# Kernel optimization log

Measured on AMD Instinct MI355X. Metric: run time of the kernel, lower is better.

Reference implementation:

```python
import jax, jax.numpy as jnp
import numpy as np

KERNEL_SIZE = 11
SIGMA = 1.5
IN_CH = 2


def _gaussian_kernel(kernel_size: int, sigma: float) -> jnp.ndarray:
    start = (1 - kernel_size) / 2
    coords = jnp.arange(start, start + kernel_size, dtype=jnp.float32)
    k1d = jnp.exp(-((coords / sigma) ** 2) / 2)
    k1d = k1d / k1d.sum()
    k2d = jnp.outer(k1d, k1d)  # [K, K]
    # OIHW depthwise kernel: [out_ch=IN_CH, in_ch/groups=1, K, K]
    return jnp.broadcast_to(k2d, (IN_CH, 1, kernel_size, kernel_size))


def _blur(img: jnp.ndarray, kernel: jnp.ndarray) -> jnp.ndarray:
    pad = KERNEL_SIZE // 2
    return jax.lax.conv_general_dilated(
        img, kernel,
        window_strides=(1, 1),
        padding=[(pad, pad), (pad, pad)],
        dimension_numbers=("NCHW", "OIHW", "NCHW"),
        feature_group_count=IN_CH,
    )


def setup_inputs() -> dict:
    key = jax.random.key(0)
    kx, ky = jax.random.split(key)
    shape = (32, 2, 512, 512)
    x = jax.random.uniform(kx, shape, dtype=jnp.float32)
    y = jax.random.uniform(ky, shape, dtype=jnp.float32)
    return {"x": x, "y": y}


def reference(x, y):
    kernel = _gaussian_kernel(KERNEL_SIZE, SIGMA)
    ux = _blur(x, kernel)
    uy = _blur(y, kernel)
    uxx = _blur(x * x, kernel)
    uyy = _blur(y * y, kernel)
    uxy = _blur(x * y, kernel)

    vx = uxx - ux * ux
    vy = uyy - uy * uy
    vxy = uxy - ux * uy

    c1 = 0.01 ** 2
    c2 = 0.03 ** 2
    numerator = (2 * ux * uy + c1) * (2 * vxy + c2)
    denominator = (ux ** 2 + uy ** 2 + c1) * (vx + vy + c2)
    ssim_map = numerator / (denominator + 1e-12)
    # as_loss=True path
    return 1 - ssim_map.mean()
```

## Files before the change

kernel.cpp:

```cpp
#include <hip/hip_runtime.h>
#include <hip/hip_fp16.h>

#define KSZ 11
#define RS 64
#define GH 13
#define ROWB 512
#define THREADS 256
#define NCHUNK 8

#define W0 1.0283800e-03f
#define W1 7.5987000e-03f
#define W2 3.6000800e-02f
#define W3 1.0936070e-01f
#define W4 2.1300550e-01f
#define W5 2.6601170e-01f

struct Pix8   { __half2 hx, hy; };
struct Pix8x2 { __half2 hx0, hy0, hx1, hy1; };
struct Pix16  { __half2 s0, s1, s2, s3; };

#define HBCOL(g, j) ((((g) + 2 * (j)) & 7) | ((j) << 3))

static __device__ __forceinline__ __half2 pkrtz(float a, float b) {
    auto v = __builtin_amdgcn_cvt_pkrtz(a, b);
    __half2 r;
    __builtin_memcpy(&r, &v, 4);
    return r;
}

static __device__ __forceinline__ void stage_load(
    const float* __restrict__ x, const float* __restrict__ y,
    size_t base0, size_t base1, int q, int g, int tileC, bool colInt,
    float2 rx0[3], float2 rx1[3], float2 ry0[3], float2 ry1[3])
{
    const int c0 = 6 * g;
    if (colInt && q < 512) {
        const size_t goff = (size_t)q * 512 + (size_t)(tileC - 8 + c0);
        const float2* X0 = (const float2*)(x + base0 + goff);
        const float2* X1 = (const float2*)(x + base1 + goff);
        const float2* Y0 = (const float2*)(y + base0 + goff);
        const float2* Y1 = (const float2*)(y + base1 + goff);
#pragma unroll
        for (int m = 0; m < 3; ++m) {
            rx0[m] = X0[m]; rx1[m] = X1[m];
            ry0[m] = Y0[m]; ry1[m] = Y1[m];
        }
    } else {
#pragma unroll
        for (int m = 0; m < 3; ++m) {
            float2 a0 = {0.f, 0.f}, a1 = {0.f, 0.f};
            float2 b0 = {0.f, 0.f}, b1 = {0.f, 0.f};
#pragma unroll
            for (int e = 0; e < 2; ++e) {
                const int gc = tileC - 8 + c0 + 2 * m + e;
                if (q >= 0 && q < 512 && gc >= 0 && gc < 512) {
                    const size_t gg = (size_t)q * 512 + (size_t)gc;
                    if (e == 0) { a0.x = x[base0+gg]; a1.x = x[base1+gg];
                                  b0.x = y[base0+gg]; b1.x = y[base1+gg]; }
                    else        { a0.y = x[base0+gg]; a1.y = x[base1+gg];
                                  b0.y = y[base0+gg]; b1.y = y[base1+gg]; }
                }
            }
            rx0[m] = a0; rx1[m] = a1; ry0[m] = b0; ry1[m] = b1;
        }
    }
}

static __device__ __forceinline__ void stage_write(
    int g, int s, Pix8* lin,
    const float2 rx0[3], const float2 rx1[3],
    const float2 ry0[3], const float2 ry1[3])
{
    const int c0 = 6 * g;
    Pix8x2* dst = (Pix8x2*)&lin[s * 64 + c0];
#pragma unroll
    for (int m = 0; m < 3; ++m) {
        Pix8x2 o;
        o.hx0 = pkrtz(rx0[m].x, rx1[m].x);
        o.hy0 = pkrtz(ry0[m].x, ry1[m].x);
        o.hx1 = pkrtz(rx0[m].y, rx1[m].y);
        o.hy1 = pkrtz(ry0[m].y, ry1[m].y);
        dst[m] = o;
    }
}

static __device__ __forceinline__ void h_item(
    int g, int s, Pix8* lin, Pix16* hb, const __half2* w2, __half2 hz)
{
    const int c0 = g << 2;
    __half2 wx[16], wy[16];
    const Pix8x2* src = (const Pix8x2*)&lin[s * 64 + (c0 + 2)];
#pragma unroll
    for (int k = 0; k < 8; ++k) {
        Pix8x2 u = src[k];
        wx[2*k]   = u.hx0; wy[2*k]   = u.hy0;
        wx[2*k+1] = u.hx1; wy[2*k+1] = u.hy1;
    }
    __half2 pp[16], qq[16];
#pragma unroll
    for (int k = 1; k < 15; ++k) {
        pp[k] = __hfma2(wy[k], wy[k], __hmul2(wx[k], wx[k]));
        qq[k] = __hmul2(wx[k], wy[k]);
    }
    __half2 s0[4] = {hz, hz, hz, hz}, s1[4] = {hz, hz, hz, hz};
    __half2 s2[4] = {hz, hz, hz, hz}, s3[4] = {hz, hz, hz, hz};
#pragma unroll
    for (int k = 1; k < 15; ++k) {
#pragma unroll
        for (int j = 0; j < 4; ++j) {
            const int tt = k - 1 - j;
            if (tt >= 0 && tt < KSZ) {
                s0[j] = __hfma2(w2[tt], wx[k], s0[j]);
                s1[j] = __hfma2(w2[tt], wy[k], s1[j]);
                s2[j] = __hfma2(w2[tt], pp[k], s2[j]);
                s3[j] = __hfma2(w2[tt], qq[k], s3[j]);
            }
        }
    }
    Pix16* orow = &hb[s * 32];
#pragma unroll
    for (int j = 0; j < 4; ++j) {
        Pix16 v;
        v.s0 = s0[j]; v.s1 = s1[j]; v.s2 = s2[j]; v.s3 = s3[j];
        orow[HBCOL(g, j)] = v;
    }
    if (s < GH) {
        Pix16* orow2 = orow + RS * 32;
#pragma unroll
        for (int j = 0; j < 4; ++j) {
            Pix16 v;
            v.s0 = s0[j]; v.s1 = s1[j]; v.s2 = s2[j]; v.s3 = s3[j];
            orow2[HBCOL(g, j)] = v;
        }
    }
}

__global__ __launch_bounds__(THREADS) void ssim_roll_kernel(
    const float* __restrict__ x, const float* __restrict__ y,
    float* __restrict__ partial)
{
    __shared__ __align__(16) unsigned char smem[(RS + GH) * ROWB];
    __shared__ float wsum[THREADS / 64];
    Pix8*  lin = (Pix8*)smem;
    Pix16* hb  = (Pix16*)smem;

    const __half2 w2[KSZ] = {
        __float2half2_rn(W0), __float2half2_rn(W1), __float2half2_rn(W2),
        __float2half2_rn(W3), __float2half2_rn(W4), __float2half2_rn(W5),
        __float2half2_rn(W4), __float2half2_rn(W3), __float2half2_rn(W2),
        __float2half2_rn(W1), __float2half2_rn(W0)};
    const __half2 hz = __float2half2_rn(0.0f);

    const int tid = threadIdx.x;
    const int bx = blockIdx.x;
    const int t  = ((bx & 7) << 2) | (bx >> 3);
    const int sx = t & 15;
    const int sg = t >> 4;
    const int B  = sg << 8;
    const int tileC = sx << 5;
    const bool colInt = (sx > 0) && (sx < 15);
    const size_t plane = 512 * 512;
    const size_t base0 = (size_t)blockIdx.y * 2 * plane;
    const size_t base1 = base0 + plane;

    {
        const int pro_q = B - 5 + (tid >> 3);
        const int pro_g = tid & 7;
        const int pro_s = (pro_q + RS) & 63;
        if (tid < 80) {
            if (pro_q >= 0) {
                float2 rx0[3], rx1[3], ry0[3], ry1[3];
                stage_load(x, y, base0, base1, pro_q, pro_g, tileC, colInt,
                           rx0, rx1, ry0, ry1);
                stage_write(pro_g, pro_s, lin, rx0, rx1, ry0, ry1);
                h_item(pro_g, pro_s, lin, hb, w2, hz);
            } else {
                Pix16 z; z.s0 = hz; z.s1 = hz; z.s2 = hz; z.s3 = hz;
                Pix16* orow = &hb[pro_s * 32];
#pragma unroll
                for (int j = 0; j < 4; ++j) orow[HBCOL(pro_g, j)] = z;
            }
        }
    }

    float bsum = 0.f;
    const int st_ro = tid >> 3, st_g = tid & 7;
    const int v_c = tid & 31, v_rg = tid >> 5;
    const int pc = HBCOL(v_c >> 2, v_c & 3);
    const __half2 c1h  = __float2half2_rn(1.0e-4f);
    const __half2 c2h  = __float2half2_rn(9.0e-4f);
    const __half2 twoh = __float2half2_rn(2.0f);

    float2 rx0[3], rx1[3], ry0[3], ry1[3];
    stage_load(x, y, base0, base1, B + 5 + st_ro, st_g, tileC, colInt,
               rx0, rx1, ry0, ry1);

#pragma unroll 1
    for (int n = 0; n < NCHUNK; ++n) {
        __syncthreads();
        const int q = B + (n << 5) + 5 + st_ro;
        const int s = q & 63;
        stage_write(st_g, s, lin, rx0, rx1, ry0, ry1);
        if (n < NCHUNK - 1)
            stage_load(x, y, base0, base1, q + 32, st_g, tileC, colInt,
                       rx0, rx1, ry0, ry1);
        h_item(st_g, s, lin, hb, w2, hz);
        __syncthreads();

        const int sb = (B + (n << 5) + (v_rg << 2) - 5 + RS) & 63;
        const Pix16* colp = &hb[sb * 32 + pc];

        __half2 b0[4] = {hz, hz, hz, hz}, b1[4] = {hz, hz, hz, hz};
        __half2 b2[4] = {hz, hz, hz, hz}, b3[4] = {hz, hz, hz, hz};
#pragma unroll
        for (int k = 0; k < 14; ++k) {
            Pix16 u = colp[k * 32];
#pragma unroll
            for (int j = 0; j < 4; ++j) {
                const int tt = k - j;
                if (tt >= 0 && tt < KSZ) {
                    b0[j] = __hfma2(w2[tt], u.s0, b0[j]);
                    b1[j] = __hfma2(w2[tt], u.s1, b1[j]);
                    b2[j] = __hfma2(w2[tt], u.s2, b2[j]);
                    b3[j] = __hfma2(w2[tt], u.s3, b3[j]);
                }
            }
        }
        __half2 acc2 = hz;
#pragma unroll
        for (int j = 0; j < 4; ++j) {
            __half2 ux = b0[j], uy = b1[j], up = b2[j], uq = b3[j];
            __half2 uxuy  = __hmul2(ux, uy);
            __half2 sumsq = __hfma2(ux, ux, __hmul2(uy, uy));
            __half2 vsum  = __hsub2(up, sumsq);
            __half2 vxy   = __hsub2(uq, uxuy);
            __half2 num   = __hmul2(__hfma2(twoh, uxuy, c1h),
                                    __hfma2(twoh, vxy, c2h));
            __half2 den   = __hmul2(__hadd2(sumsq, c1h), __hadd2(vsum, c2h));
            acc2 = __hfma2(num, h2rcp(den), acc2);
        }
        float2 af = __half22float2(acc2);
        bsum += af.x + af.y;
    }

#pragma unroll
    for (int off = 32; off > 0; off >>= 1) bsum += __shfl_down(bsum, off, 64);
    const int lane = tid & 63, wid = tid >> 6;
    if (lane == 0) wsum[wid] = bsum;
    __syncthreads();
    if (tid == 0) {
        float tot = 0.f;
#pragma unroll
        for (int i = 0; i < THREADS / 64; ++i) tot += wsum[i];
        partial[(size_t)blockIdx.y * gridDim.x + blockIdx.x] = tot;
    }
}

__global__ __launch_bounds__(256) void ssim_reduce_kernel(
    const float* __restrict__ partial, int n, float* __restrict__ out,
    double inv_count)
{
    __shared__ double ws[4];
    const float4* p4 = (const float4*)partial;
    const int n4 = n >> 2;
    double s = 0.0;
    for (int i = threadIdx.x; i < n4; i += 256) {
        float4 v = p4[i];
        s += (double)v.x + (double)v.y + (double)v.z + (double)v.w;
    }
#pragma unroll
    for (int off = 32; off > 0; off >>= 1) s += __shfl_down(s, off, 64);
    int lane = threadIdx.x & 63, wid = threadIdx.x >> 6;
    if (lane == 0) ws[wid] = s;
    __syncthreads();
    if (threadIdx.x == 0) {
        double tot = ws[0] + ws[1] + ws[2] + ws[3];
        out[0] = (float)(1.0 - tot * inv_count);
    }
}

extern "C" void kernel_launch(void* const* d_in, const int* in_sizes, int n_in,
                              void* d_out, int out_size, void* d_ws, size_t ws_size,
                              hipStream_t stream) {
    const float* x = (const float*)d_in[0];
    const float* y = (const float*)d_in[1];
    float* partial = (float*)d_ws;

    const int N = 32;
    dim3 grid(32, N);
    ssim_roll_kernel<<<grid, THREADS, 0, stream>>>(x, y, partial);

    const int nPartial = 32 * N;
    const double inv_count = 1.0 / ((double)N * 2 * 512 * 512);
    ssim_reduce_kernel<<<1, 256, 0, stream>>>(partial, nPartial, (float*)d_out,
                                              inv_count);
}
```

Baseline: 69.02 us.

## Halve row-strip height, shrink ring buffer to 48 rows, rotate staging rows

Each block now covers 128 rows instead of 256, so the grid doubles to 64x32 blocks and the reduction takes twice as many partials. The shared-memory ring shrinks from 64 to 48 rows (modulo indexing), which cuts LDS per block and should let more blocks reside per CU. A per-row rotation offset is added to the raw staging buffer to spread LDS bank accesses, and the first global load is hoisted ahead of the prologue. The cost is more halo rows recomputed per block, plus modulo arithmetic in place of masks.

New measurement: 66.77 us. 1.03x faster.

```diff
diff --git a/kernel.cpp b/kernel.cpp
--- a/kernel.cpp
+++ b/kernel.cpp
@@ -2,11 +2,11 @@
 #include <hip/hip_fp16.h>
 
 #define KSZ 11
-#define RS 64
+#define RMOD 48
 #define GH 13
 #define ROWB 512
 #define THREADS 256
-#define NCHUNK 8
+#define NCHUNK 4
 
 #define W0 1.0283800e-03f
 #define W1 7.5987000e-03f
@@ -67,12 +67,12 @@
 }
 
 static __device__ __forceinline__ void stage_write(
-    int g, int s, Pix8* lin,
+    int g, int s, int rot, Pix8* lin,
     const float2 rx0[3], const float2 rx1[3],
     const float2 ry0[3], const float2 ry1[3])
 {
     const int c0 = 6 * g;
-    Pix8x2* dst = (Pix8x2*)&lin[s * 64 + c0];
+    Pix8x2* dst = (Pix8x2*)&lin[s * 64 + c0 + rot];
 #pragma unroll
     for (int m = 0; m < 3; ++m) {
         Pix8x2 o;
@@ -85,11 +85,11 @@
 }
 
 static __device__ __forceinline__ void h_item(
-    int g, int s, Pix8* lin, Pix16* hb, const __half2* w2, __half2 hz)
+    int g, int s, int rot, Pix8* lin, Pix16* hb, const __half2* w2, __half2 hz)
 {
     const int c0 = g << 2;
     __half2 wx[16], wy[16];
-    const Pix8x2* src = (const Pix8x2*)&lin[s * 64 + (c0 + 2)];
+    const Pix8x2* src = (const Pix8x2*)&lin[s * 64 + (c0 + 2) + rot];
 #pragma unroll
     for (int k = 0; k < 8; ++k) {
         Pix8x2 u = src[k];
@@ -125,7 +125,7 @@
         orow[HBCOL(g, j)] = v;
     }
     if (s < GH) {
-        Pix16* orow2 = orow + RS * 32;
+        Pix16* orow2 = orow + RMOD * 32;
 #pragma unroll
         for (int j = 0; j < 4; ++j) {
             Pix16 v;
@@ -139,7 +139,7 @@
     const float* __restrict__ x, const float* __restrict__ y,
     float* __restrict__ partial)
 {
-    __shared__ __align__(16) unsigned char smem[(RS + GH) * ROWB];
+    __shared__ __align__(16) unsigned char smem[(RMOD + GH) * ROWB];
     __shared__ float wsum[THREADS / 64];
     Pix8*  lin = (Pix8*)smem;
     Pix16* hb  = (Pix16*)smem;
@@ -153,27 +153,34 @@
 
     const int tid = threadIdx.x;
     const int bx = blockIdx.x;
-    const int t  = ((bx & 7) << 2) | (bx >> 3);
-    const int sx = t & 15;
-    const int sg = t >> 4;
-    const int B  = sg << 8;
+    const int t  = ((bx & 7) << 3) | (bx >> 3);
+    const int sx = t >> 2;
+    const int sg = t & 3;
+    const int B  = sg << 7;
     const int tileC = sx << 5;
     const bool colInt = (sx > 0) && (sx < 15);
     const size_t plane = 512 * 512;
     const size_t base0 = (size_t)blockIdx.y * 2 * plane;
     const size_t base1 = base0 + plane;
 
+    const int st_ro = tid >> 3, st_g = tid & 7;
+
+    float2 rx0[3], rx1[3], ry0[3], ry1[3];
+    stage_load(x, y, base0, base1, B + 5 + st_ro, st_g, tileC, colInt,
+               rx0, rx1, ry0, ry1);
+
     {
         const int pro_q = B - 5 + (tid >> 3);
         const int pro_g = tid & 7;
-        const int pro_s = (pro_q + RS) & 63;
+        const int pro_s = (pro_q + 480) % RMOD;
+        const int pro_rot = (pro_s & 7) << 1;
         if (tid < 80) {
             if (pro_q >= 0) {
-                float2 rx0[3], rx1[3], ry0[3], ry1[3];
+                float2 px0[3], px1[3], py0[3], py1[3];
                 stage_load(x, y, base0, base1, pro_q, pro_g, tileC, colInt,
-                           rx0, rx1, ry0, ry1);
-                stage_write(pro_g, pro_s, lin, rx0, rx1, ry0, ry1);
-                h_item(pro_g, pro_s, lin, hb, w2, hz);
+                           px0, px1, py0, py1);
+                stage_write(pro_g, pro_s, pro_rot, lin, px0, px1, py0, py1);
+                h_item(pro_g, pro_s, pro_rot, lin, hb, w2, hz);
             } else {
                 Pix16 z; z.s0 = hz; z.s1 = hz; z.s2 = hz; z.s3 = hz;
                 Pix16* orow = &hb[pro_s * 32];
@@ -184,30 +191,26 @@
     }
 
     float bsum = 0.f;
-    const int st_ro = tid >> 3, st_g = tid & 7;
     const int v_c = tid & 31, v_rg = tid >> 5;
     const int pc = HBCOL(v_c >> 2, v_c & 3);
     const __half2 c1h  = __float2half2_rn(1.0e-4f);
     const __half2 c2h  = __float2half2_rn(9.0e-4f);
     const __half2 twoh = __float2half2_rn(2.0f);
 
-    float2 rx0[3], rx1[3], ry0[3], ry1[3];
-    stage_load(x, y, base0, base1, B + 5 + st_ro, st_g, tileC, colInt,
-               rx0, rx1, ry0, ry1);
-
 #pragma unroll 1
     for (int n = 0; n < NCHUNK; ++n) {
         __syncthreads();
         const int q = B + (n << 5) + 5 + st_ro;
-        const int s = q & 63;
-        stage_write(st_g, s, lin, rx0, rx1, ry0, ry1);
+        const int s = q % RMOD;
+        const int rot = (s & 7) << 1;
+        stage_write(st_g, s, rot, lin, rx0, rx1, ry0, ry1);
         if (n < NCHUNK - 1)
             stage_load(x, y, base0, base1, q + 32, st_g, tileC, colInt,
                        rx0, rx1, ry0, ry1);
-        h_item(st_g, s, lin, hb, w2, hz);
+        h_item(st_g, s, rot, lin, hb, w2, hz);
         __syncthreads();
 
-        const int sb = (B + (n << 5) + (v_rg << 2) - 5 + RS) & 63;
+        const int sb = (B + (n << 5) + (v_rg << 2) - 5 + 480) % RMOD;
         const Pix16* colp = &hb[sb * 32 + pc];
 
         __half2 b0[4] = {hz, hz, hz, hz}, b1[4] = {hz, hz, hz, hz};
@@ -287,10 +290,10 @@
     float* partial = (float*)d_ws;
 
     const int N = 32;
-    dim3 grid(32, N);
+    dim3 grid(64, N);
     ssim_roll_kernel<<<grid, THREADS, 0, stream>>>(x, y, partial);
 
-    const int nPartial = 32 * N;
+    const int nPartial = 64 * N;
     const double inv_count = 1.0 / ((double)N * 2 * 512 * 512);
     ssim_reduce_kernel<<<1, 256, 0, stream>>>(partial, nPartial, (float*)d_out,
                                               inv_count);
```
